# Performance work log

Hardware: AMD Instinct MI355X
Metric: run time of the kernel (lower is better)

## Reference

```python
import jax, jax.numpy as jnp
import numpy as np

B, S, L_TXT, L_IMG = 8, 4096, 77, 16
D, C, H = 1280, 2048, 20
DH = D // H
SCALE_ID, SCALE_HAIR = 1.0, 1.0


def setup_inputs() -> dict:
    key = jax.random.key(0)
    ks = jax.random.split(key, 13)
    w = lambda k, shp: jax.random.normal(k, shp, jnp.float32) * 0.02
    return dict(
        hidden_states=jax.random.normal(ks[0], (B, S, D), jnp.float32),
        text_states=jax.random.normal(ks[1], (B, L_TXT, C), jnp.float32),
        id_states=jax.random.normal(ks[2], (B, L_IMG, C), jnp.float32),
        hair_states=jax.random.normal(ks[3], (B, L_IMG, C), jnp.float32),
        Wq=w(ks[4], (D, D)),
        Wk=w(ks[5], (C, D)),
        Wv=w(ks[6], (C, D)),
        Wo=w(ks[7], (D, D)),
        bo=jnp.zeros((D,), jnp.float32),
        Wk_id=w(ks[8], (C, D)),
        Wv_id=w(ks[9], (C, D)),
        Wk_hair=w(ks[10], (C, D)),
        Wv_hair=w(ks[11], (C, D)),
    )


def reference(hidden_states, text_states, id_states, hair_states,
              Wq, Wk, Wv, Wo, bo, Wk_id, Wv_id, Wk_hair, Wv_hair):
    scale = 1.0 / jnp.sqrt(jnp.float32(DH))
    # query projection, shared across all three branches (as in the module)
    q = (hidden_states @ Wq).reshape(B, S, H, DH)  # [B,S,H,dh]

    def branch(states, Wk_, Wv_):
        k = (states @ Wk_).reshape(B, -1, H, DH)  # [B,L,H,dh]
        v = (states @ Wv_).reshape(B, -1, H, DH)
        # fp32 softmax attention (attn_fp32=True; everything already fp32)
        scores = jnp.einsum('bqhd,bkhd->bhqk', q, k) * scale
        p = jax.nn.softmax(scores, axis=-1)
        o = jnp.einsum('bhqk,bkhd->bqhd', p, v).reshape(B, S, D)
        # to_out[0] linear (shared output proj), to_out[1] dropout = identity at eval
        return o @ Wo + bo

    out = branch(text_states, Wk, Wv)
    out = out + SCALE_ID * branch(id_states, Wk_id, Wv_id)
    out = out + SCALE_HAIR * branch(hair_states, Wk_hair, Wv_hair)
    return out
```

## Files before the change

kernel.cpp:

```cpp
#include <hip/hip_runtime.h>
#include <cstdint>
#include <cstddef>

#define BB    8
#define SS    4096
#define DD    1280
#define CC    2048
#define HH    20
#define DH    64
#define LTXT  77
#define LIMG  16
#define MQ    (BB * SS)
#define MTXT  (BB * LTXT)
#define MIMG  (BB * LIMG)

typedef unsigned short u16;
typedef __bf16 bf16x8 __attribute__((ext_vector_type(8)));
typedef unsigned short u16x8 __attribute__((ext_vector_type(8)));
typedef unsigned short u16x4 __attribute__((ext_vector_type(4)));
typedef float f32x4 __attribute__((ext_vector_type(4)));

#define MFMA_BF16(a, b, c) __builtin_amdgcn_mfma_f32_16x16x32_bf16((a), (b), (c), 0, 0, 0)

__device__ __forceinline__ u16 f2bf(float f) {
  union { float f; uint32_t u; } v; v.f = f;
  return (u16)((v.u + 0x7FFFu + ((v.u >> 16) & 1u)) >> 16);
}

__device__ __forceinline__ bf16x8 ld_bf8(const u16* p) {
  return __builtin_bit_cast(bf16x8, *(const u16x8*)p);
}

__device__ __forceinline__ void async16(const void* g, void* l) {
  __builtin_amdgcn_global_load_lds(
      (__attribute__((address_space(1))) void*)(uintptr_t)g,
      (__attribute__((address_space(3))) void*)(uintptr_t)l,
      16, 0, 0);
}

__global__ void prep_kernel(
    const float* __restrict__ hidden, const float* __restrict__ txt,
    const float* __restrict__ ids, const float* __restrict__ hair,
    const float* __restrict__ Wq, const float* __restrict__ Wk,
    const float* __restrict__ Wv, const float* __restrict__ Wo,
    const float* __restrict__ Wk_id, const float* __restrict__ Wv_id,
    const float* __restrict__ Wk_hair, const float* __restrict__ Wv_hair,
    u16* __restrict__ hiddenB, u16* __restrict__ WqT, u16* __restrict__ WoT,
    u16* __restrict__ WkvTt, u16* __restrict__ WkvTi, u16* __restrict__ WkvTh,
    u16* __restrict__ stT, u16* __restrict__ stI, u16* __restrict__ stH)
{
  const int seg = blockIdx.y;
  const int64_t i0 = (int64_t)blockIdx.x * blockDim.x + threadIdx.x;
  const int64_t stride = (int64_t)gridDim.x * blockDim.x;

  switch (seg) {
    case 0: {
      const float4* src = (const float4*)hidden;
      u16x4* dst = (u16x4*)hiddenB;
      const int64_t n4 = (int64_t)MQ * DD / 4;
      for (int64_t i = i0; i < n4; i += stride) {
        float4 v = src[i];
        u16x4 o; o.x = f2bf(v.x); o.y = f2bf(v.y); o.z = f2bf(v.z); o.w = f2bf(v.w);
        dst[i] = o;
      }
      break;
    }
    case 1: {
      const int64_t n = (int64_t)DD * DD;
      for (int64_t i = i0; i < n; i += stride) {
        int nn = (int)(i / DD), kk = (int)(i - (int64_t)nn * DD);
        WqT[i] = f2bf(Wq[(int64_t)kk * DD + nn]);
      }
      break;
    }
    case 2: {
      const int64_t n = (int64_t)DD * DD;
      for (int64_t i = i0; i < n; i += stride) {
        int nn = (int)(i / DD), kk = (int)(i - (int64_t)nn * DD);
        WoT[i] = f2bf(Wo[(int64_t)kk * DD + nn]);
      }
      break;
    }
    case 3: case 4: case 5: case 6: case 7: case 8: {
      const float* W = (seg == 3) ? Wk : (seg == 4) ? Wv : (seg == 5) ? Wk_id :
                       (seg == 6) ? Wv_id : (seg == 7) ? Wk_hair : Wv_hair;
      u16* out = (seg <= 4) ? WkvTt : (seg <= 6) ? WkvTi : WkvTh;
      const int64_t halfOff = (seg == 4 || seg == 6 || seg == 8) ? (int64_t)DD * CC : 0;
      const int64_t n = (int64_t)DD * CC;
      for (int64_t i = i0; i < n; i += stride) {
        int nn = (int)(i >> 11), kk = (int)(i & 2047);
        out[halfOff + i] = f2bf(W[(int64_t)kk * DD + nn]);
      }
      break;
    }
    case 9: {
      const int64_t n = (int64_t)MTXT * CC;
      for (int64_t i = i0; i < n; i += stride) stT[i] = f2bf(txt[i]);
      break;
    }
    case 10: {
      const int64_t n = (int64_t)MIMG * CC;
      for (int64_t i = i0; i < n; i += stride) stI[i] = f2bf(ids[i]);
      break;
    }
    default: {
      const int64_t n = (int64_t)MIMG * CC;
      for (int64_t i = i0; i < n; i += stride) stH[i] = f2bf(hair[i]);
      break;
    }
  }
}

template<int OUT_MODE>
__device__ __forceinline__ void gemm_tile_body(
    const u16* __restrict__ A, const u16* __restrict__ Bt, void* __restrict__ Cv,
    int M, int N, int K, int tm, int tn,
    float outScale, const float* __restrict__ bias, float biasScale)
{
  __shared__ u16 As[128 * 32];
  __shared__ u16 Bs[128 * 32];

  const int tid = threadIdx.x;
  const int w  = tid >> 6;
  const int l  = tid & 63;
  const int q4 = l >> 4;
  const int lm = l & 15;
  const int wM = w & 1;
  const int wN = w >> 1;

  int rA0 = tm * 128 + w * 32 + (l >> 2);
  int rA1 = rA0 + 16;
  if (rA0 > M - 1) rA0 = M - 1;
  if (rA1 > M - 1) rA1 = M - 1;
  const int cc = (l & 3) * 8;
  const u16* gA0 = A + (size_t)rA0 * K + cc;
  const u16* gA1 = A + (size_t)rA1 * K + cc;
  const int rB = tn * 128 + w * 32 + (l >> 2);
  const u16* gB0 = Bt + (size_t)rB * K + cc;
  const u16* gB1 = gB0 + (size_t)16 * K;
  u16* lA0 = As + (w * 32) * 32;
  u16* lA1 = As + (w * 32 + 16) * 32;
  u16* lB0 = Bs + (w * 32) * 32;
  u16* lB1 = Bs + (w * 32 + 16) * 32;

  f32x4 acc[4][4] = {};

  for (int k0 = 0; k0 < K; k0 += 32) {
    async16(gA0, lA0);
    async16(gA1, lA1);
    async16(gB0, lB0);
    async16(gB1, lB1);
    gA0 += 32; gA1 += 32; gB0 += 32; gB1 += 32;
    __syncthreads();
    bf16x8 af[4], bfr[4];
#pragma unroll
    for (int i = 0; i < 4; i++) {
      af[i]  = ld_bf8(As + (wM * 64 + i * 16 + lm) * 32 + q4 * 8);
      bfr[i] = ld_bf8(Bs + (wN * 64 + i * 16 + lm) * 32 + q4 * 8);
    }
#pragma unroll
    for (int i = 0; i < 4; i++)
#pragma unroll
      for (int j = 0; j < 4; j++)
        acc[i][j] = MFMA_BF16(af[i], bfr[j], acc[i][j]);
    __syncthreads();
  }

  if constexpr (OUT_MODE == 0) {
    u16* C = (u16*)Cv;
#pragma unroll
    for (int i = 0; i < 4; i++)
#pragma unroll
      for (int r = 0; r < 4; r++) {
        const int row = tm * 128 + wM * 64 + i * 16 + q4 * 4 + r;
        if (row < M) {
          u16* cp = C + (size_t)row * N + tn * 128 + wN * 64 + lm;
#pragma unroll
          for (int j = 0; j < 4; j++)
            cp[j * 16] = f2bf(acc[i][j][r] * outScale);
        }
      }
  } else {
    float* C = (float*)Cv;
    float bs[4];
#pragma unroll
    for (int j = 0; j < 4; j++)
      bs[j] = biasScale * bias[tn * 128 + wN * 64 + j * 16 + lm];
#pragma unroll
    for (int i = 0; i < 4; i++)
#pragma unroll
      for (int r = 0; r < 4; r++) {
        const int row = tm * 128 + wM * 64 + i * 16 + q4 * 4 + r;
        if (row < M) {
          float* cp = C + (size_t)row * N + tn * 128 + wN * 64 + lm;
#pragma unroll
          for (int j = 0; j < 4; j++)
            cp[j * 16] = acc[i][j][r] + bs[j];
        }
      }
  }
}

__global__ __launch_bounds__(256, 2) void gemm_bf16_out(
    const u16* __restrict__ A, const u16* __restrict__ Bt, u16* __restrict__ C,
    int M, int N, int K, float scale)
{
  gemm_tile_body<0>(A, Bt, C, M, N, K, blockIdx.x, blockIdx.y, scale, nullptr, 0.f);
}

__global__ __launch_bounds__(256, 2) void gemm_f32_bias(
    const u16* __restrict__ A, const u16* __restrict__ Bt, float* __restrict__ C,
    int M, int N, int K, const float* __restrict__ bias, float biasScale)
{
  gemm_tile_body<1>(A, Bt, C, M, N, K, blockIdx.x, blockIdx.y, 1.f, bias, biasScale);
}

__global__ __launch_bounds__(256, 2) void gemm_kv3(
    const u16* A0, const u16* A1, const u16* A2,
    const u16* B0, const u16* B1, const u16* B2,
    u16* C0, u16* C1, u16* C2, int M0, int M1, int M2)
{
  const int z = blockIdx.z;
  const u16* A  = (z == 0) ? A0 : (z == 1) ? A1 : A2;
  const u16* Bt = (z == 0) ? B0 : (z == 1) ? B1 : B2;
  u16* C        = (z == 0) ? C0 : (z == 1) ? C1 : C2;
  const int M   = (z == 0) ? M0 : (z == 1) ? M1 : M2;
  if ((int)blockIdx.x * 128 >= M) return;
  gemm_tile_body<0>(A, Bt, C, M, 2 * DD, CC, blockIdx.x, blockIdx.y, 1.f, nullptr, 0.f);
}

constexpr int KS  = 72;
constexpr int VST = 104;
constexpr int VSI = 40;
constexpr int PS  = 104;

template<int NT, int L, int KP, int VS>
__device__ __forceinline__ void attn_branch(
    const u16* __restrict__ Klds, const u16* __restrict__ Vlds, u16* __restrict__ Pw,
    const bf16x8& qf0, const bf16x8& qf1, int lm, int q4, f32x4* acc)
{
  f32x4 sc[NT];
#pragma unroll
  for (int nt = 0; nt < NT; nt++) {
    f32x4 c = {};
    c = MFMA_BF16(qf0, ld_bf8(Klds + (nt * 16 + lm) * KS + q4 * 8), c);
    c = MFMA_BF16(qf1, ld_bf8(Klds + (nt * 16 + lm) * KS + 32 + q4 * 8), c);
    sc[nt] = c;
  }
  float mx[4] = {-3e38f, -3e38f, -3e38f, -3e38f};
#pragma unroll
  for (int nt = 0; nt < NT; nt++) {
    const bool valid = (nt * 16 + lm) < L;
#pragma unroll
    for (int r = 0; r < 4; r++)
      if (valid) mx[r] = fmaxf(mx[r], sc[nt][r]);
  }
#pragma unroll
  for (int r = 0; r < 4; r++) {
    mx[r] = fmaxf(mx[r], __shfl_xor(mx[r], 1));
    mx[r] = fmaxf(mx[r], __shfl_xor(mx[r], 2));
    mx[r] = fmaxf(mx[r], __shfl_xor(mx[r], 4));
    mx[r] = fmaxf(mx[r], __shfl_xor(mx[r], 8));
  }
  float sm[4] = {0.f, 0.f, 0.f, 0.f};
#pragma unroll
  for (int nt = 0; nt < NT; nt++) {
    const bool valid = (nt * 16 + lm) < L;
#pragma unroll
    for (int r = 0; r < 4; r++) {
      float e = valid ? __expf(sc[nt][r] - mx[r]) : 0.f;
      sc[nt][r] = e;
      sm[r] += e;
    }
  }
#pragma unroll
  for (int r = 0; r < 4; r++) {
    sm[r] += __shfl_xor(sm[r], 1);
    sm[r] += __shfl_xor(sm[r], 2);
    sm[r] += __shfl_xor(sm[r], 4);
    sm[r] += __shfl_xor(sm[r], 8);
  }
  float inv[4];
#pragma unroll
  for (int r = 0; r < 4; r++) inv[r] = 1.0f / sm[r];
#pragma unroll
  for (int nt = 0; nt < NT; nt++)
#pragma unroll
    for (int r = 0; r < 4; r++)
      Pw[(q4 * 4 + r) * PS + nt * 16 + lm] = f2bf(sc[nt][r] * inv[r]);
  if (NT * 16 < KP) {
#pragma unroll
    for (int r = 0; r < 4; r++)
      Pw[(q4 * 4 + r) * PS + NT * 16 + lm] = 0;
  }
  __syncthreads();
#pragma unroll
  for (int kt = 0; kt < KP / 32; kt++) {
    const bf16x8 af = ld_bf8(Pw + lm * PS + kt * 32 + q4 * 8);
#pragma unroll
    for (int d = 0; d < 4; d++)
      acc[d] = MFMA_BF16(af, ld_bf8(Vlds + (d * 16 + lm) * VS + kt * 32 + q4 * 8), acc[d]);
  }
  __syncthreads();
}

__global__ __launch_bounds__(256, 2) void attn_kernel(
    const u16* __restrict__ Qb, const u16* __restrict__ kvT,
    const u16* __restrict__ kvI, const u16* __restrict__ kvH,
    u16* __restrict__ Ob)
{
  __shared__ u16 Kt[80 * KS];
  __shared__ u16 Vt[64 * VST];
  __shared__ u16 Ki[16 * KS];
  __shared__ u16 Kh[16 * KS];
  __shared__ u16 Vi[64 * VSI];
  __shared__ u16 Vh[64 * VSI];
  __shared__ u16 Pl[4][16 * PS];

  const int qt = blockIdx.x, h = blockIdx.y, b = blockIdx.z;
  const int tid = threadIdx.x;
  const int w  = tid >> 6;
  const int l  = tid & 63;
  const int q4 = l >> 4;
  const int lm = l & 15;

  for (int i = tid; i < 80 * 64; i += 256) {
    const int key = i >> 6, dh = i & 63;
    Kt[key * KS + dh] = (key < LTXT)
        ? kvT[((size_t)(b * LTXT + key)) * (2 * DD) + h * 64 + dh] : (u16)0;
  }
  for (int i = tid; i < 64 * 96; i += 256) {
    const int dh = i / 96, key = i % 96;
    Vt[dh * VST + key] = (key < LTXT)
        ? kvT[((size_t)(b * LTXT + key)) * (2 * DD) + DD + h * 64 + dh] : (u16)0;
  }
  for (int i = tid; i < 16 * 64; i += 256) {
    const int key = i >> 6, dh = i & 63;
    Ki[key * KS + dh] = kvI[((size_t)(b * LIMG + key)) * (2 * DD) + h * 64 + dh];
    Kh[key * KS + dh] = kvH[((size_t)(b * LIMG + key)) * (2 * DD) + h * 64 + dh];
  }
  for (int i = tid; i < 64 * 32; i += 256) {
    const int dh = i >> 5, key = i & 31;
    Vi[dh * VSI + key] = (key < LIMG)
        ? kvI[((size_t)(b * LIMG + key)) * (2 * DD) + DD + h * 64 + dh] : (u16)0;
    Vh[dh * VSI + key] = (key < LIMG)
        ? kvH[((size_t)(b * LIMG + key)) * (2 * DD) + DD + h * 64 + dh] : (u16)0;
  }
  for (int i = tid; i < 16 * PS; i += 256) {
    Pl[0][i] = 0; Pl[1][i] = 0; Pl[2][i] = 0; Pl[3][i] = 0;
  }
  __syncthreads();

  const int srow = qt * 64 + w * 16 + lm;
  const u16* qp = Qb + ((size_t)(b * SS + srow)) * DD + h * 64 + q4 * 8;
  const bf16x8 qf0 = ld_bf8(qp);
  const bf16x8 qf1 = ld_bf8(qp + 32);

  f32x4 acc[4] = {};

  attn_branch<5, LTXT, 96, VST>(Kt, Vt, Pl[w], qf0, qf1, lm, q4, acc);
  attn_branch<1, LIMG, 32, VSI>(Ki, Vi, Pl[w], qf0, qf1, lm, q4, acc);
  attn_branch<1, LIMG, 32, VSI>(Kh, Vh, Pl[w], qf0, qf1, lm, q4, acc);

#pragma unroll
  for (int d = 0; d < 4; d++)
#pragma unroll
    for (int r = 0; r < 4; r++) {
      const int row = qt * 64 + w * 16 + q4 * 4 + r;
      Ob[((size_t)(b * SS + row)) * DD + h * 64 + d * 16 + lm] = f2bf(acc[d][r]);
    }
}

extern "C" void kernel_launch(void* const* d_in, const int* in_sizes, int n_in,
                              void* d_out, int out_size, void* d_ws, size_t ws_size,
                              hipStream_t stream) {
  (void)in_sizes; (void)n_in; (void)out_size; (void)ws_size;
  const float* hidden  = (const float*)d_in[0];
  const float* txt     = (const float*)d_in[1];
  const float* ids     = (const float*)d_in[2];
  const float* hair    = (const float*)d_in[3];
  const float* Wq      = (const float*)d_in[4];
  const float* Wk      = (const float*)d_in[5];
  const float* Wv      = (const float*)d_in[6];
  const float* Wo      = (const float*)d_in[7];
  const float* bo      = (const float*)d_in[8];
  const float* Wk_id   = (const float*)d_in[9];
  const float* Wv_id   = (const float*)d_in[10];
  const float* Wk_hair = (const float*)d_in[11];
  const float* Wv_hair = (const float*)d_in[12];
  float* out = (float*)d_out;

  char* ws = (char*)d_ws;
  size_t off = 0;
  auto alloc = [&](size_t bytes) {
    void* p = ws + off;
    off = (off + bytes + 255) & ~(size_t)255;
    return p;
  };
  u16* hiddenB = (u16*)alloc((size_t)MQ * DD * 2);
  u16* QB      = (u16*)alloc((size_t)MQ * DD * 2);
  u16* OB      = (u16*)alloc((size_t)MQ * DD * 2);
  u16* WqT     = (u16*)alloc((size_t)DD * DD * 2);
  u16* WoT     = (u16*)alloc((size_t)DD * DD * 2);
  u16* WkvTt   = (u16*)alloc((size_t)2 * DD * CC * 2);
  u16* WkvTi   = (u16*)alloc((size_t)2 * DD * CC * 2);
  u16* WkvTh   = (u16*)alloc((size_t)2 * DD * CC * 2);
  u16* stT     = (u16*)alloc((size_t)MTXT * CC * 2);
  u16* stI     = (u16*)alloc((size_t)MIMG * CC * 2);
  u16* stH     = (u16*)alloc((size_t)MIMG * CC * 2);
  u16* kvT     = (u16*)alloc((size_t)MTXT * 2 * DD * 2);
  u16* kvI     = (u16*)alloc((size_t)MIMG * 2 * DD * 2);
  u16* kvH     = (u16*)alloc((size_t)MIMG * 2 * DD * 2);

  prep_kernel<<<dim3(1024, 12), 256, 0, stream>>>(
      hidden, txt, ids, hair, Wq, Wk, Wv, Wo, Wk_id, Wv_id, Wk_hair, Wv_hair,
      hiddenB, WqT, WoT, WkvTt, WkvTi, WkvTh, stT, stI, stH);

  gemm_bf16_out<<<dim3(MQ / 128, DD / 128), 256, 0, stream>>>(
      hiddenB, WqT, QB, MQ, DD, DD, 0.125f);

  gemm_kv3<<<dim3((MTXT + 127) / 128, (2 * DD) / 128, 3), 256, 0, stream>>>(
      stT, stI, stH, WkvTt, WkvTi, WkvTh, kvT, kvI, kvH, MTXT, MIMG, MIMG);

  attn_kernel<<<dim3(SS / 64, HH, BB), 256, 0, stream>>>(QB, kvT, kvI, kvH, OB);

  gemm_f32_bias<<<dim3(MQ / 128, DD / 128), 256, 0, stream>>>(
      OB, WoT, out, MQ, DD, DD, bo, 3.0f);
}
```

Measured before the change: 1.033 ms.

## Amortize attention K/V staging over 256 queries per block, vectorize loads, drop barriers

Each attention block now loops over four 16-row query tiles per wave, 256 queries in total, so the per-(batch, head) K/V staging into LDS is shared by four times as many queries. The staging loops now use 8-wide vector global loads instead of scalar element loads. The redundant zeroing of the probability buffer is dropped. The per-branch __syncthreads are removed, relying on each wave owning its own P buffer. The cost is four times fewer blocks, which lowers parallelism across the grid, and correctness now depends on in-wave LDS ordering for P.

```diff
diff --git a/kernel.cpp b/kernel.cpp
--- a/kernel.cpp
+++ b/kernel.cpp
@@ -293,7 +293,6 @@
     for (int r = 0; r < 4; r++)
       Pw[(q4 * 4 + r) * PS + NT * 16 + lm] = 0;
   }
-  __syncthreads();
 #pragma unroll
   for (int kt = 0; kt < KP / 32; kt++) {
     const bf16x8 af = ld_bf8(Pw + lm * PS + kt * 32 + q4 * 8);
@@ -301,7 +300,6 @@
     for (int d = 0; d < 4; d++)
       acc[d] = MFMA_BF16(af, ld_bf8(Vlds + (d * 16 + lm) * VS + kt * 32 + q4 * 8), acc[d]);
   }
-  __syncthreads();
 }
 
 __global__ __launch_bounds__(256, 2) void attn_kernel(
@@ -319,56 +317,71 @@
 
   const int qt = blockIdx.x, h = blockIdx.y, b = blockIdx.z;
   const int tid = threadIdx.x;
+
+  for (int i = tid; i < 640; i += 256) {
+    const int key = i >> 3, g = i & 7;
+    u16x8 v = {};
+    if (key < LTXT)
+      v = *(const u16x8*)(kvT + (size_t)(b * LTXT + key) * (2 * DD) + h * 64 + g * 8);
+    *(u16x8*)(Kt + key * KS + g * 8) = v;
+  }
+  {
+    const int i = tid;
+    const int which = i >> 7, j = i & 127;
+    const int key = j >> 3, g = j & 7;
+    const u16* src = which ? kvH : kvI;
+    u16* dst = which ? Kh : Ki;
+    *(u16x8*)(dst + key * KS + g * 8) =
+        *(const u16x8*)(src + (size_t)(b * LIMG + key) * (2 * DD) + h * 64 + g * 8);
+  }
+  for (int i = tid; i < 768; i += 256) {
+    const int key = i >> 3, g = i & 7;
+    u16x8 v = {};
+    if (key < LTXT)
+      v = *(const u16x8*)(kvT + (size_t)(b * LTXT + key) * (2 * DD) + DD + h * 64 + g * 8);
+#pragma unroll
+    for (int j = 0; j < 8; j++) Vt[(g * 8 + j) * VST + key] = v[j];
+  }
+  for (int i = tid; i < 512; i += 256) {
+    const int which = i >> 8, j2 = i & 255;
+    const int key = j2 >> 3, g = j2 & 7;
+    const u16* src = which ? kvH : kvI;
+    u16* dst = which ? Vh : Vi;
+    u16x8 v = {};
+    if (key < LIMG)
+      v = *(const u16x8*)(src + (size_t)(b * LIMG + key) * (2 * DD) + DD + h * 64 + g * 8);
+#pragma unroll
+    for (int j = 0; j < 8; j++) dst[(g * 8 + j) * VSI + key] = v[j];
+  }
+  __syncthreads();
+
   const int w  = tid >> 6;
   const int l  = tid & 63;
   const int q4 = l >> 4;
   const int lm = l & 15;
-
-  for (int i = tid; i < 80 * 64; i += 256) {
-    const int key = i >> 6, dh = i & 63;
-    Kt[key * KS + dh] = (key < LTXT)
-        ? kvT[((size_t)(b * LTXT + key)) * (2 * DD) + h * 64 + dh] : (u16)0;
-  }
-  for (int i = tid; i < 64 * 96; i += 256) {
-    const int dh = i / 96, key = i % 96;
-    Vt[dh * VST + key] = (key < LTXT)
-        ? kvT[((size_t)(b * LTXT + key)) * (2 * DD) + DD + h * 64 + dh] : (u16)0;
-  }
-  for (int i = tid; i < 16 * 64; i += 256) {
-    const int key = i >> 6, dh = i & 63;
-    Ki[key * KS + dh] = kvI[((size_t)(b * LIMG + key)) * (2 * DD) + h * 64 + dh];
-    Kh[key * KS + dh] = kvH[((size_t)(b * LIMG + key)) * (2 * DD) + h * 64 + dh];
-  }
-  for (int i = tid; i < 64 * 32; i += 256) {
-    const int dh = i >> 5, key = i & 31;
-    Vi[dh * VSI + key] = (key < LIMG)
-        ? kvI[((size_t)(b * LIMG + key)) * (2 * DD) + DD + h * 64 + dh] : (u16)0;
-    Vh[dh * VSI + key] = (key < LIMG)
-        ? kvH[((size_t)(b * LIMG + key)) * (2 * DD) + DD + h * 64 + dh] : (u16)0;
-  }
-  for (int i = tid; i < 16 * PS; i += 256) {
-    Pl[0][i] = 0; Pl[1][i] = 0; Pl[2][i] = 0; Pl[3][i] = 0;
-  }
-  __syncthreads();
-
-  const int srow = qt * 64 + w * 16 + lm;
-  const u16* qp = Qb + ((size_t)(b * SS + srow)) * DD + h * 64 + q4 * 8;
-  const bf16x8 qf0 = ld_bf8(qp);
-  const bf16x8 qf1 = ld_bf8(qp + 32);
-
-  f32x4 acc[4] = {};
-
-  attn_branch<5, LTXT, 96, VST>(Kt, Vt, Pl[w], qf0, qf1, lm, q4, acc);
-  attn_branch<1, LIMG, 32, VSI>(Ki, Vi, Pl[w], qf0, qf1, lm, q4, acc);
-  attn_branch<1, LIMG, 32, VSI>(Kh, Vh, Pl[w], qf0, qf1, lm, q4, acc);
-
-#pragma unroll
-  for (int d = 0; d < 4; d++)
-#pragma unroll
-    for (int r = 0; r < 4; r++) {
-      const int row = qt * 64 + w * 16 + q4 * 4 + r;
-      Ob[((size_t)(b * SS + row)) * DD + h * 64 + d * 16 + lm] = f2bf(acc[d][r]);
-    }
+  u16* Pw = Pl[w];
+  const int qbase = qt * 256 + w * 64;
+
+#pragma unroll
+  for (int m = 0; m < 4; m++) {
+    const int qrow = qbase + m * 16;
+    const u16* qp = Qb + ((size_t)(b * SS + qrow + lm)) * DD + h * 64 + q4 * 8;
+    const bf16x8 qf0 = ld_bf8(qp);
+    const bf16x8 qf1 = ld_bf8(qp + 32);
+
+    f32x4 acc[4] = {};
+    attn_branch<5, LTXT, 96, VST>(Kt, Vt, Pw, qf0, qf1, lm, q4, acc);
+    attn_branch<1, LIMG, 32, VSI>(Ki, Vi, Pw, qf0, qf1, lm, q4, acc);
+    attn_branch<1, LIMG, 32, VSI>(Kh, Vh, Pw, qf0, qf1, lm, q4, acc);
+
+#pragma unroll
+    for (int d = 0; d < 4; d++)
+#pragma unroll
+      for (int r = 0; r < 4; r++) {
+        const int row = qrow + q4 * 4 + r;
+        Ob[((size_t)(b * SS + row)) * DD + h * 64 + d * 16 + lm] = f2bf(acc[d][r]);
+      }
+  }
 }
 
 extern "C" void kernel_launch(void* const* d_in, const int* in_sizes, int n_in,
@@ -422,7 +435,7 @@
   gemm_kv3<<<dim3((MTXT + 127) / 128, (2 * DD) / 128, 3), 256, 0, stream>>>(
       stT, stI, stH, WkvTt, WkvTi, WkvTh, kvT, kvI, kvH, MTXT, MIMG, MIMG);
 
-  attn_kernel<<<dim3(SS / 64, HH, BB), 256, 0, stream>>>(QB, kvT, kvI, kvH, OB);
+  attn_kernel<<<dim3(SS / 256, HH, BB), 256, 0, stream>>>(QB, kvT, kvI, kvH, OB);
 
   gemm_f32_bias<<<dim3(MQ / 128, DD / 128), 256, 0, stream>>>(
       OB, WoT, out, MQ, DD, DD, bo, 3.0f);
```

After: 833.0 us. -19.4%, faster.
